# Optimization experiments

Measured on AMD Instinct MI355X. Metric: run time of the kernel, lower is better.

## Reference

```python
import jax, jax.numpy as jnp
import numpy as np

H, D = 16, 64          # num_heads, head_dim
OUT = H * D            # out_dim = 1024
W1, W2 = 32, 32        # sliding windows
EPS_NORM = 1e-7
EPS_LN = 1e-5


def setup_inputs() -> dict:
    key = jax.random.key(0)
    ks = jax.random.split(key, 6)
    B, S, IN = 2, 2048, 1024
    x = jax.random.normal(ks[0], (B, S, IN), dtype=jnp.float32)
    scale = 0.02
    W_Q = jax.random.normal(ks[1], (IN, OUT), dtype=jnp.float32) * scale
    W_K = jax.random.normal(ks[2], (IN, OUT), dtype=jnp.float32) * scale
    W_V = jax.random.normal(ks[3], (IN, OUT), dtype=jnp.float32) * scale
    W_Kp = jax.random.normal(ks[4], (IN, OUT), dtype=jnp.float32) * scale
    W_O = jax.random.normal(ks[5], (OUT, OUT), dtype=jnp.float32) * scale
    ln_gamma = jnp.ones((OUT,), dtype=jnp.float32)
    ln_beta = jnp.zeros((OUT,), dtype=jnp.float32)
    return {"x": x, "W_Q": W_Q, "W_K": W_K, "W_V": W_V, "W_Kp": W_Kp,
            "W_O": W_O, "ln_gamma": ln_gamma, "ln_beta": ln_beta}


def _l2norm(t):
    return t / (jnp.linalg.norm(t, axis=-1, keepdims=True) + EPS_NORM)


def reference(x, W_Q, W_K, W_V, W_Kp, W_O, ln_gamma, ln_beta):
    B, S, _ = x.shape
    # projections -> (B, S, H, D)
    Q = _l2norm((x @ W_Q).reshape(B, S, H, D))
    K = _l2norm((x @ W_K).reshape(B, S, H, D))
    Kp = _l2norm((x @ W_Kp).reshape(B, S, H, D))
    V = (x @ W_V).reshape(B, S, H, D)
    # windowed keys/values (last w1/w2 positions, as in the PyTorch fallback)
    K_win = K[:, -W1:]
    Kp_win = Kp[:, -W2:]
    V_win = V[:, -W1:]
    Vp_win = V[:, -W2:]
    # triple product A_ijk = q.k.k' / sqrt(D) -> (B, S, H, w1, w2)
    A = jnp.einsum('bshd,bjhd,bkhd->bshjk', Q, K_win, Kp_win) / jnp.sqrt(jnp.float32(D))
    # causal window mask: allow j <= i + w1 - S and k <= i + w2 - S
    s_idx = jnp.arange(S)[:, None, None]
    j_idx = jnp.arange(W1)[None, :, None]
    k_idx = jnp.arange(W2)[None, None, :]
    mask = (j_idx > s_idx + (W1 - S)) | (k_idx > s_idx + (W2 - S))  # (S, w1, w2)
    neg_inf = jnp.float32(-jnp.inf)
    A = jnp.where(mask[None, :, None, :, :], neg_inf, A)
    # joint softmax over (j, k); fully-masked query rows produce zeros
    A_flat = A.reshape(B, S, H, W1 * W2)
    all_masked = jnp.all(A_flat == neg_inf, axis=-1, keepdims=True)
    A_safe = jnp.where(all_masked, 0.0, A_flat)
    P = jax.nn.softmax(A_safe, axis=-1)
    P = jnp.where(all_masked, 0.0, P).reshape(B, S, H, W1, W2)
    # value outer-product weighting (V' = V)
    Z = jnp.einsum('bshjk,bjhd,bkhd->bshd', P, V_win, Vp_win)
    out = Z.reshape(B, S, OUT) @ W_O
    out = out + x  # residual (shapes match)
    # LayerNorm
    mu = jnp.mean(out, axis=-1, keepdims=True)
    var = jnp.mean((out - mu) ** 2, axis=-1, keepdims=True)
    out = (out - mu) / jnp.sqrt(var + EPS_LN) * ln_gamma + ln_beta
    return out
```

## Files before the change

### kernel.cpp

```cpp
#include <hip/hip_runtime.h>
#include <math.h>


#define XS 68

#define YQ_OFF    0
#define YK_OFF    65536
#define YKP_OFF   131072
#define YV_OFF    196608
#define Z_OFF     262144
#define DELTA_OFF 327680
#define WS_FLOATS 393216

__global__ __launch_bounds__(256) void zero_ws(float4* __restrict__ ws) {
  ws[blockIdx.x * 256 + threadIdx.x] = make_float4(0.f, 0.f, 0.f, 0.f);
}

__global__ __launch_bounds__(256, 4) void proj_kernel(
    const float* __restrict__ x,
    const float* __restrict__ Wq, const float* __restrict__ Wk,
    const float* __restrict__ Wkp, const float* __restrict__ Wv,
    float* __restrict__ Y) {
  __shared__ float xs[64 * 65];
  const int tid = threadIdx.x;
  const int z    = blockIdx.x >> 4;
  const int col0 = (blockIdx.x & 15) * 64;
  const int k0   = blockIdx.y * 64;
  const float* __restrict__ W =
      (z == 0) ? Wq : ((z == 1) ? Wk : ((z == 2) ? Wkp : Wv));

  #pragma unroll
  for (int i = 0; i < 4; i++) {
    int e = i * 256 + tid;
    int r = e >> 4, q = e & 15;
    int b = r >> 5, t = r & 31;
    float4 v = *(const float4*)(x + ((b * 2048 + 2016 + t) * 1024 + k0 + q * 4));
    xs[(q * 4 + 0) * 65 + r] = v.x;
    xs[(q * 4 + 1) * 65 + r] = v.y;
    xs[(q * 4 + 2) * 65 + r] = v.z;
    xs[(q * 4 + 3) * 65 + r] = v.w;
  }
  __syncthreads();

  const int wave = __builtin_amdgcn_readfirstlane(tid >> 6);
  const int lane = tid & 63;
  const float* __restrict__ Wt = W + (size_t)k0 * 1024 + col0 + wave * 16;

  float acc[16];
  #pragma unroll
  for (int c = 0; c < 16; c++) acc[c] = 0.f;

  #pragma unroll 4
  for (int kk = 0; kk < 64; kk++) {
    float xv = xs[kk * 65 + lane];
    const float* __restrict__ wrow = Wt + kk * 1024;
    #pragma unroll
    for (int c = 0; c < 16; c++) acc[c] = fmaf(xv, wrow[c], acc[c]);
  }

  __syncthreads();
  #pragma unroll
  for (int c = 0; c < 16; c++) xs[lane * 65 + wave * 16 + c] = acc[c];
  __syncthreads();
  float* __restrict__ Yo = Y + z * 65536 + col0;
  #pragma unroll
  for (int i = 0; i < 16; i++) {
    int r = wave * 16 + i;
    atomicAdd(Yo + r * 1024 + lane, xs[r * 65 + lane]);
  }
}

__global__ __launch_bounds__(256) void attn_kernel(
    const float* __restrict__ Y, float* __restrict__ Zout) {
  __shared__ float Kn[32 * XS], Kp[32 * XS], Vs[32 * XS];
  __shared__ float Pt[4][32 * 33];
  __shared__ float qs[4][64];
  const int tid = threadIdx.x;
  const int wave = tid >> 6, lane = tid & 63;
  const int h = blockIdx.y, b = blockIdx.z;

  #pragma unroll
  for (int i = 0; i < 8; i++) {
    int e = i * 256 + tid;
    int row = e >> 6, d = e & 63;
    int src = (b * 32 + row) * 1024 + h * 64 + d;
    Kn[row * XS + d] = Y[YK_OFF + src];
    Kp[row * XS + d] = Y[YKP_OFF + src];
    Vs[row * XS + d] = Y[YV_OFF + src];
  }
  __syncthreads();

  for (int rr = 0; rr < 8; rr++) {
    int row = wave * 8 + rr;
    float kv = Kn[row * XS + lane];
    float s2 = kv * kv;
    #pragma unroll
    for (int off = 1; off < 64; off <<= 1) s2 += __shfl_xor(s2, off);
    Kn[row * XS + lane] = kv * (1.f / (sqrtf(s2) + 1e-7f));
    float pv = Kp[row * XS + lane];
    float p2 = pv * pv;
    #pragma unroll
    for (int off = 1; off < 64; off <<= 1) p2 += __shfl_xor(p2, off);
    Kp[row * XS + lane] = pv * (1.f / (sqrtf(p2) + 1e-7f));
  }
  __syncthreads();

  const int m = blockIdx.x * 4 + wave;
  const int r = b * 32 + m;

  float q = Y[YQ_OFF + r * 1024 + h * 64 + lane];
  float q2 = q * q;
  #pragma unroll
  for (int off = 1; off < 64; off <<= 1) q2 += __shfl_xor(q2, off);
  q *= (1.f / (sqrtf(q2) + 1e-7f));
  qs[wave][lane] = q;
  __builtin_amdgcn_wave_barrier();

  const int lj = lane >> 3, lk = lane & 7;
  float acc[4][4];
  #pragma unroll
  for (int a = 0; a < 4; a++)
    #pragma unroll
    for (int c = 0; c < 4; c++) acc[a][c] = 0.f;

  const float* qw = qs[wave];
  for (int dq = 0; dq < 16; dq++) {
    float4 q4 = *(const float4*)(qw + dq * 4);
    float4 t4[4], kp4[4];
    #pragma unroll
    for (int tj = 0; tj < 4; tj++) {
      float4 kv = *(const float4*)(Kn + (lj * 4 + tj) * XS + dq * 4);
      t4[tj].x = q4.x * kv.x; t4[tj].y = q4.y * kv.y;
      t4[tj].z = q4.z * kv.z; t4[tj].w = q4.w * kv.w;
    }
    #pragma unroll
    for (int tk = 0; tk < 4; tk++)
      kp4[tk] = *(const float4*)(Kp + (lk * 4 + tk) * XS + dq * 4);
    #pragma unroll
    for (int tj = 0; tj < 4; tj++)
      #pragma unroll
      for (int tk = 0; tk < 4; tk++)
        acc[tj][tk] += t4[tj].x * kp4[tk].x + t4[tj].y * kp4[tk].y
                     + t4[tj].z * kp4[tk].z + t4[tj].w * kp4[tk].w;
  }

  float amax = -1e30f;
  #pragma unroll
  for (int tj = 0; tj < 4; tj++)
    #pragma unroll
    for (int tk = 0; tk < 4; tk++) {
      int j = lj * 4 + tj, k = lk * 4 + tk;
      if (j <= m && k <= m) amax = fmaxf(amax, acc[tj][tk] * 0.125f);
    }
  #pragma unroll
  for (int off = 1; off < 64; off <<= 1) amax = fmaxf(amax, __shfl_xor(amax, off));

  float lsum = 0.f;
  float* ptw = Pt[wave];
  #pragma unroll
  for (int tj = 0; tj < 4; tj++)
    #pragma unroll
    for (int tk = 0; tk < 4; tk++) {
      int j = lj * 4 + tj, k = lk * 4 + tk;
      float e = 0.f;
      if (j <= m && k <= m) e = __expf(acc[tj][tk] * 0.125f - amax);
      lsum += e;
      ptw[k * 33 + j] = e;
    }
  #pragma unroll
  for (int off = 1; off < 64; off <<= 1) lsum += __shfl_xor(lsum, off);
  float inv = 1.f / lsum;
  __builtin_amdgcn_wave_barrier();

  float vreg[32];
  #pragma unroll
  for (int k = 0; k < 32; k++) vreg[k] = Vs[k * XS + lane];
  float zacc = 0.f;
  for (int k = 0; k <= m; k++) {
    float g = 0.f;
    #pragma unroll
    for (int j = 0; j < 32; j++) g += ptw[k * 33 + j] * vreg[j];
    zacc += g * vreg[k];
  }
  Zout[r * 1024 + h * 64 + lane] = zacc * inv;
}

__global__ __launch_bounds__(256, 4) void wo_kernel(
    const float* __restrict__ Zr, const float* __restrict__ Wo,
    float* __restrict__ delta) {
  __shared__ float xs[64 * 65];
  const int tid = threadIdx.x;
  const int col0 = blockIdx.x * 64;
  const int k0   = blockIdx.y * 32;

  #pragma unroll
  for (int i = 0; i < 2; i++) {
    int e = i * 256 + tid;
    int r = e >> 3, q = e & 7;
    float4 v = *(const float4*)(Zr + r * 1024 + k0 + q * 4);
    xs[(q * 4 + 0) * 65 + r] = v.x;
    xs[(q * 4 + 1) * 65 + r] = v.y;
    xs[(q * 4 + 2) * 65 + r] = v.z;
    xs[(q * 4 + 3) * 65 + r] = v.w;
  }
  __syncthreads();

  const int wave = __builtin_amdgcn_readfirstlane(tid >> 6);
  const int lane = tid & 63;
  const float* __restrict__ Wt = Wo + (size_t)k0 * 1024 + col0 + wave * 16;

  float acc[16];
  #pragma unroll
  for (int c = 0; c < 16; c++) acc[c] = 0.f;

  #pragma unroll 4
  for (int kk = 0; kk < 32; kk++) {
    float xv = xs[kk * 65 + lane];
    const float* __restrict__ wrow = Wt + kk * 1024;
    #pragma unroll
    for (int c = 0; c < 16; c++) acc[c] = fmaf(xv, wrow[c], acc[c]);
  }

  __syncthreads();
  #pragma unroll
  for (int c = 0; c < 16; c++) xs[lane * 65 + wave * 16 + c] = acc[c];
  __syncthreads();
  #pragma unroll
  for (int i = 0; i < 16; i++) {
    int r = wave * 16 + i;
    atomicAdd(delta + r * 1024 + col0 + lane, xs[r * 65 + lane]);
  }
}

__global__ __launch_bounds__(256, 4) void ln_kernel(
    const float4* __restrict__ x4, const float4* __restrict__ delta4,
    const float4* __restrict__ g4, const float4* __restrict__ b4,
    float4* __restrict__ out4) {
  const int tid = threadIdx.x;
  const int wave = tid >> 6, lane = tid & 63;
  const int row = blockIdx.x * 4 + wave;
  const int b = row >> 11, s = row & 2047;

  float4 v[4];
  #pragma unroll
  for (int i = 0; i < 4; i++) v[i] = x4[row * 256 + i * 64 + lane];
  if (s >= 2016) {
    int drow = b * 32 + (s - 2016);
    #pragma unroll
    for (int i = 0; i < 4; i++) {
      float4 d = delta4[drow * 256 + i * 64 + lane];
      v[i].x += d.x; v[i].y += d.y; v[i].z += d.z; v[i].w += d.w;
    }
  }
  float sum = 0.f, ss = 0.f;
  #pragma unroll
  for (int i = 0; i < 4; i++) {
    sum += v[i].x + v[i].y + v[i].z + v[i].w;
    ss  += v[i].x * v[i].x + v[i].y * v[i].y + v[i].z * v[i].z + v[i].w * v[i].w;
  }
  #pragma unroll
  for (int off = 1; off < 64; off <<= 1) {
    sum += __shfl_xor(sum, off);
    ss  += __shfl_xor(ss, off);
  }
  float mu   = sum * (1.f / 1024.f);
  float var  = ss * (1.f / 1024.f) - mu * mu;
  float rstd = rsqrtf(var + 1e-5f);

  #pragma unroll
  for (int i = 0; i < 4; i++) {
    float4 g = g4[i * 64 + lane];
    float4 be = b4[i * 64 + lane];
    float4 o;
    o.x = (v[i].x - mu) * rstd * g.x + be.x;
    o.y = (v[i].y - mu) * rstd * g.y + be.y;
    o.z = (v[i].z - mu) * rstd * g.z + be.z;
    o.w = (v[i].w - mu) * rstd * g.w + be.w;
    out4[row * 256 + i * 64 + lane] = o;
  }
}

extern "C" void kernel_launch(void* const* d_in, const int* in_sizes, int n_in,
                              void* d_out, int out_size, void* d_ws, size_t ws_size,
                              hipStream_t stream) {
  const float* x   = (const float*)d_in[0];
  const float* Wq  = (const float*)d_in[1];
  const float* Wk  = (const float*)d_in[2];
  const float* Wv  = (const float*)d_in[3];
  const float* Wkp = (const float*)d_in[4];
  const float* Wo  = (const float*)d_in[5];
  const float* gam = (const float*)d_in[6];
  const float* bet = (const float*)d_in[7];
  float* out = (float*)d_out;
  float* ws  = (float*)d_ws;

  hipLaunchKernelGGL(zero_ws, dim3(WS_FLOATS / 1024), dim3(256), 0, stream,
                     (float4*)ws);
  hipLaunchKernelGGL(proj_kernel, dim3(64, 16), dim3(256), 0, stream,
                     x, Wq, Wk, Wkp, Wv, ws);
  hipLaunchKernelGGL(attn_kernel, dim3(8, 16, 2), dim3(256), 0, stream,
                     ws, ws + Z_OFF);
  hipLaunchKernelGGL(wo_kernel, dim3(16, 32), dim3(256), 0, stream,
                     ws + Z_OFF, Wo, ws + DELTA_OFF);
  hipLaunchKernelGGL(ln_kernel, dim3(1024), dim3(256), 0, stream,
                     (const float4*)x, (const float4*)(ws + DELTA_OFF),
                     (const float4*)gam, (const float4*)bet, (float4*)out);
}
```

Baseline: 141.8 us.

## Replace atomic split-K reductions with partial buffers summed by consumers

The projection and output-projection GEMMs now write split-K partial results to separate workspace slices with plain stores, and the consumer kernels (attention and LayerNorm) sum those partials. This removes the workspace-zeroing kernel and the atomic adds. W tiles are now staged through shared memory with coalesced float4 loads instead of per-lane global reads. The split count drops from 16 to 8 for projections and from 32 to 16 for Wo, which reduces parallelism and adds extra partial reads in the consumers.

```diff
diff --git a/kernel.cpp b/kernel.cpp
--- a/kernel.cpp
+++ b/kernel.cpp
@@ -4,17 +4,12 @@
 
 #define XS 68
 
-#define YQ_OFF    0
-#define YK_OFF    65536
-#define YKP_OFF   131072
-#define YV_OFF    196608
-#define Z_OFF     262144
-#define DELTA_OFF 327680
-#define WS_FLOATS 393216
-
-__global__ __launch_bounds__(256) void zero_ws(float4* __restrict__ ws) {
-  ws[blockIdx.x * 256 + threadIdx.x] = make_float4(0.f, 0.f, 0.f, 0.f);
-}
+#define YP_STR   262144
+#define NKS_P    8
+#define ZF_OFF   (NKS_P * YP_STR)
+#define DP_OFF   (ZF_OFF + 65536)
+#define DP_STR   65536
+#define NKS_W    16
 
 __global__ __launch_bounds__(256, 4) void proj_kernel(
     const float* __restrict__ x,
@@ -22,51 +17,65 @@
     const float* __restrict__ Wkp, const float* __restrict__ Wv,
     float* __restrict__ Y) {
   __shared__ float xs[64 * 65];
-  const int tid = threadIdx.x;
-  const int z    = blockIdx.x >> 4;
-  const int col0 = (blockIdx.x & 15) * 64;
-  const int k0   = blockIdx.y * 64;
+  __shared__ float wl[64 * 68];
+  const int tid  = threadIdx.x;
+  const int cb   = blockIdx.x;
+  const int ks   = blockIdx.y;
+  const int col0 = cb * 64;
+  const int z    = cb >> 4;
+  const int colz = col0 & 1023;
   const float* __restrict__ W =
       (z == 0) ? Wq : ((z == 1) ? Wk : ((z == 2) ? Wkp : Wv));
 
-  #pragma unroll
-  for (int i = 0; i < 4; i++) {
-    int e = i * 256 + tid;
-    int r = e >> 4, q = e & 15;
-    int b = r >> 5, t = r & 31;
-    float4 v = *(const float4*)(x + ((b * 2048 + 2016 + t) * 1024 + k0 + q * 4));
-    xs[(q * 4 + 0) * 65 + r] = v.x;
-    xs[(q * 4 + 1) * 65 + r] = v.y;
-    xs[(q * 4 + 2) * 65 + r] = v.z;
-    xs[(q * 4 + 3) * 65 + r] = v.w;
-  }
-  __syncthreads();
-
   const int wave = __builtin_amdgcn_readfirstlane(tid >> 6);
   const int lane = tid & 63;
-  const float* __restrict__ Wt = W + (size_t)k0 * 1024 + col0 + wave * 16;
 
   float acc[16];
   #pragma unroll
   for (int c = 0; c < 16; c++) acc[c] = 0.f;
 
-  #pragma unroll 4
-  for (int kk = 0; kk < 64; kk++) {
-    float xv = xs[kk * 65 + lane];
-    const float* __restrict__ wrow = Wt + kk * 1024;
-    #pragma unroll
-    for (int c = 0; c < 16; c++) acc[c] = fmaf(xv, wrow[c], acc[c]);
-  }
-
-  __syncthreads();
+  for (int cc = 0; cc < 2; cc++) {
+    const int kb = ks * 128 + cc * 64;
+    #pragma unroll
+    for (int i = 0; i < 4; i++) {
+      int e = i * 256 + tid;
+      int r = e >> 4, q = e & 15;
+      int b = r >> 5, t = r & 31;
+      float4 v = *(const float4*)(x + ((b * 2048 + 2016 + t) * 1024 + kb + q * 4));
+      xs[(q * 4 + 0) * 65 + r] = v.x;
+      xs[(q * 4 + 1) * 65 + r] = v.y;
+      xs[(q * 4 + 2) * 65 + r] = v.z;
+      xs[(q * 4 + 3) * 65 + r] = v.w;
+    }
+    #pragma unroll
+    for (int i = 0; i < 4; i++) {
+      int e = i * 256 + tid;
+      int r = e >> 4, q = e & 15;
+      float4 v = *(const float4*)(W + (size_t)(kb + r) * 1024 + colz + q * 4);
+      float* d = wl + r * 68 + q * 4;
+      d[0] = v.x; d[1] = v.y; d[2] = v.z; d[3] = v.w;
+    }
+    __syncthreads();
+
+    const float* __restrict__ wbase = wl + wave * 16;
+    #pragma unroll 4
+    for (int kk = 0; kk < 64; kk++) {
+      float xv = xs[kk * 65 + lane];
+      const float* __restrict__ wrow = wbase + kk * 68;
+      #pragma unroll
+      for (int c = 0; c < 16; c++) acc[c] = fmaf(xv, wrow[c], acc[c]);
+    }
+    __syncthreads();
+  }
+
   #pragma unroll
   for (int c = 0; c < 16; c++) xs[lane * 65 + wave * 16 + c] = acc[c];
   __syncthreads();
-  float* __restrict__ Yo = Y + z * 65536 + col0;
+  float* __restrict__ Yo = Y + ks * YP_STR + col0;
   #pragma unroll
   for (int i = 0; i < 16; i++) {
     int r = wave * 16 + i;
-    atomicAdd(Yo + r * 1024 + lane, xs[r * 65 + lane]);
+    Yo[r * 4096 + lane] = xs[r * 65 + lane];
   }
 }
 
@@ -83,10 +92,14 @@
   for (int i = 0; i < 8; i++) {
     int e = i * 256 + tid;
     int row = e >> 6, d = e & 63;
-    int src = (b * 32 + row) * 1024 + h * 64 + d;
-    Kn[row * XS + d] = Y[YK_OFF + src];
-    Kp[row * XS + d] = Y[YKP_OFF + src];
-    Vs[row * XS + d] = Y[YV_OFF + src];
+    int src = (b * 32 + row) * 4096 + h * 64 + d;
+    float kn = 0.f, kp = 0.f, vv = 0.f;
+    #pragma unroll
+    for (int p = 0; p < NKS_P; p++) {
+      const float* Yp = Y + p * YP_STR + src;
+      kn += Yp[1024]; kp += Yp[2048]; vv += Yp[3072];
+    }
+    Kn[row * XS + d] = kn; Kp[row * XS + d] = kp; Vs[row * XS + d] = vv;
   }
   __syncthreads();
 
@@ -108,7 +121,9 @@
   const int m = blockIdx.x * 4 + wave;
   const int r = b * 32 + m;
 
-  float q = Y[YQ_OFF + r * 1024 + h * 64 + lane];
+  float q = 0.f;
+  #pragma unroll
+  for (int p = 0; p < NKS_P; p++) q += Y[p * YP_STR + r * 4096 + h * 64 + lane];
   float q2 = q * q;
   #pragma unroll
   for (int off = 1; off < 64; off <<= 1) q2 += __shfl_xor(q2, off);
@@ -187,36 +202,46 @@
 
 __global__ __launch_bounds__(256, 4) void wo_kernel(
     const float* __restrict__ Zr, const float* __restrict__ Wo,
-    float* __restrict__ delta) {
+    float* __restrict__ Dp) {
   __shared__ float xs[64 * 65];
-  const int tid = threadIdx.x;
+  __shared__ float wl[64 * 68];
+  const int tid  = threadIdx.x;
   const int col0 = blockIdx.x * 64;
-  const int k0   = blockIdx.y * 32;
-
-  #pragma unroll
-  for (int i = 0; i < 2; i++) {
+  const int ks   = blockIdx.y;
+  const int kb   = ks * 64;
+
+  const int wave = __builtin_amdgcn_readfirstlane(tid >> 6);
+  const int lane = tid & 63;
+
+  #pragma unroll
+  for (int i = 0; i < 4; i++) {
     int e = i * 256 + tid;
-    int r = e >> 3, q = e & 7;
-    float4 v = *(const float4*)(Zr + r * 1024 + k0 + q * 4);
+    int r = e >> 4, q = e & 15;
+    float4 v = *(const float4*)(Zr + r * 1024 + kb + q * 4);
     xs[(q * 4 + 0) * 65 + r] = v.x;
     xs[(q * 4 + 1) * 65 + r] = v.y;
     xs[(q * 4 + 2) * 65 + r] = v.z;
     xs[(q * 4 + 3) * 65 + r] = v.w;
   }
-  __syncthreads();
-
-  const int wave = __builtin_amdgcn_readfirstlane(tid >> 6);
-  const int lane = tid & 63;
-  const float* __restrict__ Wt = Wo + (size_t)k0 * 1024 + col0 + wave * 16;
+  #pragma unroll
+  for (int i = 0; i < 4; i++) {
+    int e = i * 256 + tid;
+    int r = e >> 4, q = e & 15;
+    float4 v = *(const float4*)(Wo + (size_t)(kb + r) * 1024 + col0 + q * 4);
+    float* d = wl + r * 68 + q * 4;
+    d[0] = v.x; d[1] = v.y; d[2] = v.z; d[3] = v.w;
+  }
+  __syncthreads();
 
   float acc[16];
   #pragma unroll
   for (int c = 0; c < 16; c++) acc[c] = 0.f;
 
+  const float* __restrict__ wbase = wl + wave * 16;
   #pragma unroll 4
-  for (int kk = 0; kk < 32; kk++) {
+  for (int kk = 0; kk < 64; kk++) {
     float xv = xs[kk * 65 + lane];
-    const float* __restrict__ wrow = Wt + kk * 1024;
+    const float* __restrict__ wrow = wbase + kk * 68;
     #pragma unroll
     for (int c = 0; c < 16; c++) acc[c] = fmaf(xv, wrow[c], acc[c]);
   }
@@ -225,15 +250,16 @@
   #pragma unroll
   for (int c = 0; c < 16; c++) xs[lane * 65 + wave * 16 + c] = acc[c];
   __syncthreads();
+  float* __restrict__ D = Dp + ks * DP_STR + col0;
   #pragma unroll
   for (int i = 0; i < 16; i++) {
     int r = wave * 16 + i;
-    atomicAdd(delta + r * 1024 + col0 + lane, xs[r * 65 + lane]);
+    D[r * 1024 + lane] = xs[r * 65 + lane];
   }
 }
 
 __global__ __launch_bounds__(256, 4) void ln_kernel(
-    const float4* __restrict__ x4, const float4* __restrict__ delta4,
+    const float4* __restrict__ x4, const float4* __restrict__ dp4,
     const float4* __restrict__ g4, const float4* __restrict__ b4,
     float4* __restrict__ out4) {
   const int tid = threadIdx.x;
@@ -247,9 +273,12 @@
   if (s >= 2016) {
     int drow = b * 32 + (s - 2016);
     #pragma unroll
-    for (int i = 0; i < 4; i++) {
-      float4 d = delta4[drow * 256 + i * 64 + lane];
-      v[i].x += d.x; v[i].y += d.y; v[i].z += d.z; v[i].w += d.w;
+    for (int p = 0; p < NKS_W; p++) {
+      #pragma unroll
+      for (int i = 0; i < 4; i++) {
+        float4 d = dp4[p * 16384 + drow * 256 + i * 64 + lane];
+        v[i].x += d.x; v[i].y += d.y; v[i].z += d.z; v[i].w += d.w;
+      }
     }
   }
   float sum = 0.f, ss = 0.f;
@@ -294,15 +323,13 @@
   float* out = (float*)d_out;
   float* ws  = (float*)d_ws;
 
-  hipLaunchKernelGGL(zero_ws, dim3(WS_FLOATS / 1024), dim3(256), 0, stream,
-                     (float4*)ws);
-  hipLaunchKernelGGL(proj_kernel, dim3(64, 16), dim3(256), 0, stream,
+  hipLaunchKernelGGL(proj_kernel, dim3(64, NKS_P), dim3(256), 0, stream,
                      x, Wq, Wk, Wkp, Wv, ws);
   hipLaunchKernelGGL(attn_kernel, dim3(8, 16, 2), dim3(256), 0, stream,
-                     ws, ws + Z_OFF);
-  hipLaunchKernelGGL(wo_kernel, dim3(16, 32), dim3(256), 0, stream,
-                     ws + Z_OFF, Wo, ws + DELTA_OFF);
+                     ws, ws + ZF_OFF);
+  hipLaunchKernelGGL(wo_kernel, dim3(16, NKS_W), dim3(256), 0, stream,
+                     ws + ZF_OFF, Wo, ws + DP_OFF);
   hipLaunchKernelGGL(ln_kernel, dim3(1024), dim3(256), 0, stream,
-                     (const float4*)x, (const float4*)(ws + DELTA_OFF),
+                     (const float4*)x, (const float4*)(ws + DP_OFF),
                      (const float4*)gam, (const float4*)bet, (float4*)out);
 }
```

New measurement: 136.4 us. 1.04x faster.
